# Kernel tuning notes

Measured on AMD Instinct MI355X. Metric: run time of the kernel, lower is better.

## Reference

```python
import jax, jax.numpy as jnp
import numpy as np

B, N, H = 8, 128, 512   # batch, num_sent (n == m required by the 'all' branch), hidden_size
D = 2 * H               # bi-LSTM output dim
SCALE = 0.05


def setup_inputs() -> dict:
    key = jax.random.key(0)
    ks = jax.random.split(key, 24)
    p = lambda k, shape: (jax.random.normal(k, shape, dtype=jnp.float32) * SCALE)
    return {
        "x0_enc": jax.random.normal(ks[0], (B, N, D), dtype=jnp.float32),
        "x1_enc": jax.random.normal(ks[1], (B, N, D), dtype=jnp.float32),
        # concat_attention
        "Wc1": p(ks[2], (D, H)), "Wc2": p(ks[3], (D, H)), "vc": p(ks[4], (H,)),
        # bilinear_attention
        "Wb": p(ks[5], (D, D)),
        # dot_attention x2 (separate params)
        "Wd1": p(ks[6], (D, H)), "vd1": p(ks[7], (H,)),
        "Wd2": p(ks[8], (D, H)), "vd2": p(ks[9], (H,)),
        # minus_attention (Ws/vs are unused in forward)
        "Wm": p(ks[10], (D, H)), "vm": p(ks[11], (H,)),
        # aggregation_layer
        "Wq": p(ks[12], (D, H)), "vq": p(ks[13], (H,)),
        "Wp1": p(ks[14], (2 * D, H)), "Wp2": p(ks[15], (D, H)), "vp": p(ks[16], (H,)),
        "Wpred": p(ks[17], (2 * D, 2)), "bpred": jnp.zeros((2,), dtype=jnp.float32),
    }


def _dot_att(x, y, Wd, vd):
    # sjt[b,m,n] = vd . tanh(Wd(x[b,n] * y[b,m]))  -- pairwise elementwise product + MLP
    z = jnp.tanh(jnp.einsum("bnd,bmd,dh->bmnh", x, y, Wd))  # [B,m,n,H]
    s = jnp.einsum("bmnh,h->bmn", z, vd)
    a = jax.nn.softmax(s, axis=2)
    return jnp.einsum("bmn,bnd->bmd", a, x)


def _minus_att(x, y, Wm, vm):
    # Wm is linear, so Wm(x_n - y_m) = (x@Wm)_n - (y@Wm)_m
    a, b = x @ Wm, y @ Wm                                    # [B,n,H], [B,m,H]
    z = jnp.tanh(a[:, None, :, :] - b[:, :, None, :])        # [B,m,n,H]
    s = jnp.einsum("bmnh,h->bmn", z, vm)
    att = jax.nn.softmax(s, axis=2)
    return jnp.einsum("bmn,bnd->bmd", att, x)


def _concat_att(x, y, Wc1, Wc2, vc):
    a, b = x @ Wc1, y @ Wc2                                  # [B,n,H], [B,m,H]
    z = jnp.tanh(a[:, None, :, :] + b[:, :, None, :])        # [B,m,n,H]
    s = jnp.einsum("bmnh,h->bmn", z, vc)
    att = jax.nn.softmax(s, axis=2)
    return jnp.einsum("bmn,bnd->bmd", att, x)


def _bilinear_att(x, y, Wb):
    s = jnp.einsum("bmd,bnd->bmn", y, x @ Wb)
    att = jax.nn.softmax(s, axis=2)
    return jnp.einsum("bmn,bnd->bmd", att, x)


def reference(x0_enc, x1_enc, Wc1, Wc2, vc, Wb, Wd1, vd1, Wd2, vd2, Wm, vm,
              Wq, vq, Wp1, Wp2, vp, Wpred, bpred):
    x0, x1 = x0_enc, x1_enc
    # attention_fx('all')
    qtc = _concat_att(x0, x1, Wc1, Wc2, vc)
    qtb = _bilinear_att(x0, x1, Wb)
    qts = _dot_att(x0, x1, Wd1, vd1)
    qtd = _dot_att(x1, x0, Wd2, vd2)
    qtm = _minus_att(x0, x1, Wm, vm)
    agg_res = jnp.max(jnp.stack([x1, qts, qtc, qtd, qtb, qtm], axis=0), axis=0)  # [B,m,2H]
    # MultiAtt: dropout is identity in eval
    agg_rep = jnp.concatenate([x1, agg_res], axis=2)                             # [B,m,4H]
    # aggregation_layer
    sj = jnp.einsum("bnh,h->bn", jnp.tanh(x0 @ Wq), vq)
    rq = jnp.einsum("bn,bnd->bd", jax.nn.softmax(sj, axis=1), x0)                # [B,2H]
    t = agg_rep @ Wp1 + (rq @ Wp2)[:, None, :]                                   # [B,m,H]
    sp = jax.nn.softmax(jnp.einsum("bmh,h->bm", t, vp), axis=1)
    rp = jnp.einsum("bm,bmd->bd", sp, agg_rep)                                   # [B,4H]
    out = jax.nn.relu(rp @ Wpred + bpred)                                        # [B,2]
    return out
```

## Files before the change

kernel.cpp:

```cpp
#include <hip/hip_runtime.h>
#include <hip/hip_bf16.h>

static constexpr int Bc = 8, Nc = 128, Dc = 1024, Hc = 512;
static constexpr int BM = Bc * Nc;

typedef short short8 __attribute__((ext_vector_type(8)));
typedef float floatx4 __attribute__((ext_vector_type(4)));

__device__ __forceinline__ float fast_tanh(float x) {
  x = fminf(fmaxf(x, -15.f), 15.f);
  float e = __expf(2.f * x);
  return (e - 1.f) / (e + 1.f);
}

__device__ __forceinline__ ushort f2bf(float f) {
  unsigned u = __float_as_uint(f);
  u += 0x7FFFu + ((u >> 16) & 1u);
  return (ushort)(u >> 16);
}

__device__ __forceinline__ unsigned pk2(float a, float b) {
  return (unsigned)f2bf(a) | ((unsigned)f2bf(b) << 16);
}

__device__ __forceinline__ float block_sum256(float v, float* buf4) {
  #pragma unroll
  for (int o = 32; o; o >>= 1) v += __shfl_down(v, o, 64);
  const int w = threadIdx.x >> 6, lane = threadIdx.x & 63;
  if (lane == 0) buf4[w] = v;
  __syncthreads();
  return buf4[0] + buf4[1] + buf4[2] + buf4[3];
}

__global__ __launch_bounds__(256) void cvt_both(const float* __restrict__ x0,
                                                const float* __restrict__ x1,
                                                ushort* __restrict__ o0,
                                                ushort* __restrict__ o1) {
  int bi = blockIdx.x;
  const float* src = (bi < 512) ? x0 : x1;
  ushort* dst = (bi < 512) ? o0 : o1;
  int off = (bi & 511);
  int i = (off * 256 + threadIdx.x) * 8;
  float4 a = *reinterpret_cast<const float4*>(&src[i]);
  float4 b = *reinterpret_cast<const float4*>(&src[i + 4]);
  uint4 o;
  o.x = pk2(a.x, a.y); o.y = pk2(a.z, a.w);
  o.z = pk2(b.x, b.y); o.w = pk2(b.z, b.w);
  *reinterpret_cast<uint4*>(&dst[i]) = o;
}

struct TJobs {
  const float* src[7];
  ushort* dst[7];
  int J[7];
};
__global__ __launch_bounds__(256) void conv_transpose_multi(TJobs jobs) {
  const int job = blockIdx.z;
  const int J = jobs.J[job];
  const int h0 = blockIdx.y * 64;
  if (h0 >= J) return;
  const float* W = jobs.src[job];
  ushort* WT = jobs.dst[job];
  __shared__ float tile[64][65];
  const int d0 = blockIdx.x * 64;
  const int tid = threadIdx.x;
  #pragma unroll
  for (int i = 0; i < 16; i++) {
    int idx = tid + i * 256;
    int dd = idx >> 6, hh = idx & 63;
    tile[dd][hh] = W[(size_t)(d0 + dd) * J + h0 + hh];
  }
  __syncthreads();
  #pragma unroll
  for (int i = 0; i < 16; i++) {
    int idx = tid + i * 256;
    int hh = idx >> 6, dd = idx & 63;
    WT[(size_t)(h0 + hh) * Dc + d0 + dd] = f2bf(tile[dd][hh]);
  }
}

__global__ __launch_bounds__(256) void gemm_bt(const ushort* __restrict__ A,
                                               const ushort* __restrict__ BT,
                                               float* __restrict__ Cf,
                                               ushort* __restrict__ Cbf,
                                               int K, int ldc,
                                               size_t sA, size_t sB, size_t sC) {
  const int bz = blockIdx.z;
  A  += (size_t)bz * sA;
  BT += (size_t)bz * sB;
  const int m0 = blockIdx.y * 64, n0 = blockIdx.x * 64;
  __shared__ __align__(16) ushort Asl[64][40];
  __shared__ __align__(16) ushort Bsl[64][40];
  const int tid = threadIdx.x, wave = tid >> 6, lane = tid & 63;
  const int quad = lane >> 4, l15 = lane & 15;
  const int wr = (wave & 1) * 32, wc = (wave >> 1) * 32;
  const int rSt = tid >> 2, kSt8 = (tid & 3) * 8;
  floatx4 acc[2][2];
  #pragma unroll
  for (int i = 0; i < 2; i++)
    #pragma unroll
    for (int j = 0; j < 2; j++) acc[i][j] = (floatx4){0.f, 0.f, 0.f, 0.f};
  uint4 pa = *reinterpret_cast<const uint4*>(&A[(size_t)(m0 + rSt) * K + kSt8]);
  uint4 pb = *reinterpret_cast<const uint4*>(&BT[(size_t)(n0 + rSt) * K + kSt8]);
  for (int k0 = 0; k0 < K; k0 += 32) {
    *reinterpret_cast<uint4*>(&Asl[rSt][kSt8]) = pa;
    *reinterpret_cast<uint4*>(&Bsl[rSt][kSt8]) = pb;
    __syncthreads();
    if (k0 + 32 < K) {
      pa = *reinterpret_cast<const uint4*>(&A[(size_t)(m0 + rSt) * K + k0 + 32 + kSt8]);
      pb = *reinterpret_cast<const uint4*>(&BT[(size_t)(n0 + rSt) * K + k0 + 32 + kSt8]);
    }
    short8 af[2], bb[2];
    #pragma unroll
    for (int i = 0; i < 2; i++)
      af[i] = *reinterpret_cast<const short8*>(&Asl[wr + i * 16 + l15][quad * 8]);
    #pragma unroll
    for (int j = 0; j < 2; j++)
      bb[j] = *reinterpret_cast<const short8*>(&Bsl[wc + j * 16 + l15][quad * 8]);
    #pragma unroll
    for (int i = 0; i < 2; i++)
      #pragma unroll
      for (int j = 0; j < 2; j++)
        acc[i][j] = __builtin_amdgcn_mfma_f32_16x16x32_bf16(af[i], bb[j], acc[i][j], 0, 0, 0);
    __syncthreads();
  }
  if (Cbf) {
    #pragma unroll
    for (int i = 0; i < 2; i++)
      #pragma unroll
      for (int j = 0; j < 2; j++)
        #pragma unroll
        for (int r = 0; r < 4; r++) {
          int row = m0 + wr + i * 16 + quad * 4 + r;
          int col = n0 + wc + j * 16 + l15;
          Cbf[(size_t)bz * sC + (size_t)row * ldc + col] = f2bf(acc[i][j][r]);
        }
  } else {
    #pragma unroll
    for (int i = 0; i < 2; i++)
      #pragma unroll
      for (int j = 0; j < 2; j++)
        #pragma unroll
        for (int r = 0; r < 4; r++) {
          int row = m0 + wr + i * 16 + quad * 4 + r;
          int col = n0 + wc + j * 16 + l15;
          Cf[(size_t)bz * sC + (size_t)row * ldc + col] = acc[i][j][r];
        }
  }
}

__global__ __launch_bounds__(256, 2) void dot_scores_mfma3(const float* __restrict__ X0,
                                                           const float* __restrict__ X1,
                                                           const ushort* __restrict__ WdT1,
                                                           const ushort* __restrict__ WdT2,
                                                           const float* __restrict__ vd1,
                                                           const float* __restrict__ vd2,
                                                           float* __restrict__ Sd) {
  const int which = blockIdx.z;
  const float* X = which ? X1 : X0;
  const float* Y = which ? X0 : X1;
  const ushort* WdT = which ? WdT2 : WdT1;
  const float* v = which ? vd2 : vd1;
  float* S = Sd + (size_t)which * (BM * Nc);

  const int bm = blockIdx.y;
  const int b = bm >> 7;
  const int hBase = blockIdx.x * 256;
  const int tid = threadIdx.x;
  const int wave = tid >> 6, lane = tid & 63;
  const int quad = lane >> 4, l15 = lane & 15;
  const int wn = wave & 1, wh = wave >> 1;

  __shared__ __align__(16) char smraw[65536];
  ushort (*As0)[40] = (ushort(*)[40])(smraw);
  ushort (*As1)[40] = (ushort(*)[40])(smraw + 10240);
  ushort (*Bs0)[40] = (ushort(*)[40])(smraw + 20480);
  ushort (*Bs1)[40] = (ushort(*)[40])(smraw + 40960);
  float* yl = (float*)(smraw + 61440);
  float (*red)[33] = (float(*)[33])(smraw);

  for (int i = tid; i < Dc; i += 256) yl[i] = Y[(size_t)bm * Dc + i];

  floatx4 acc[4][8];
  #pragma unroll
  for (int i = 0; i < 4; i++)
    #pragma unroll
    for (int j = 0; j < 8; j++) acc[i][j] = (floatx4){0.f, 0.f, 0.f, 0.f};

  const float* Xb = X + (size_t)b * Nc * Dc;
  const int nSt = tid >> 2;
  const int kSt4 = (tid & 3) * 4;
  const int kSt8 = (tid & 3) * 8;

  auto stage = [&](int k0, ushort (*Asb)[40], ushort (*Bsb)[40]) {
    #pragma unroll
    for (int u2 = 0; u2 < 4; u2++) {
      const int n = (u2 >> 1) * 64 + nSt;
      const int kc = (u2 & 1) * 16 + kSt4;
      float4 xv = *reinterpret_cast<const float4*>(&Xb[(size_t)n * Dc + k0 + kc]);
      float4 yv = *reinterpret_cast<const float4*>(&yl[k0 + kc]);
      uint2 o;
      o.x = pk2(xv.x * yv.x, xv.y * yv.y);
      o.y = pk2(xv.z * yv.z, xv.w * yv.w);
      *reinterpret_cast<uint2*>(&Asb[n][kc]) = o;
    }
    #pragma unroll
    for (int r = 0; r < 4; r++)
      *reinterpret_cast<uint4*>(&Bsb[r * 64 + nSt][kSt8]) =
          *reinterpret_cast<const uint4*>(&WdT[(size_t)(hBase + r * 64 + nSt) * Dc + k0 + kSt8]);
  };

  auto mfma_step = [&](ushort (*Asb)[40], ushort (*Bsb)[40]) {
    short8 af[4], bfr[8];
    #pragma unroll
    for (int i = 0; i < 4; i++)
      af[i] = *reinterpret_cast<const short8*>(&Asb[wn * 64 + i * 16 + l15][quad * 8]);
    #pragma unroll
    for (int j = 0; j < 8; j++)
      bfr[j] = *reinterpret_cast<const short8*>(&Bsb[wh * 128 + j * 16 + l15][quad * 8]);
    #pragma unroll
    for (int i = 0; i < 4; i++)
      #pragma unroll
      for (int j = 0; j < 8; j++)
        acc[i][j] = __builtin_amdgcn_mfma_f32_16x16x32_bf16(af[i], bfr[j], acc[i][j], 0, 0, 0);
  };

  __syncthreads();
  stage(0, As0, Bs0);
  __syncthreads();
  #pragma unroll 1
  for (int s = 0; s < 32; s += 2) {
    if (s + 1 < 32) stage((s + 1) * 32, As1, Bs1);
    mfma_step(As0, Bs0);
    __syncthreads();
    if (s + 2 < 32) stage((s + 2) * 32, As0, Bs0);
    mfma_step(As1, Bs1);
    __syncthreads();
  }

  float vv[8];
  #pragma unroll
  for (int j = 0; j < 8; j++) vv[j] = v[hBase + wh * 128 + j * 16 + l15];
  #pragma unroll
  for (int i = 0; i < 4; i++)
    #pragma unroll
    for (int r = 0; r < 4; r++) {
      float p = 0.f;
      #pragma unroll
      for (int j = 0; j < 8; j++) p = fmaf(vv[j], fast_tanh(acc[i][j][r]), p);
      red[wn * 64 + i * 16 + quad * 4 + r][wh * 16 + l15] = p;
    }
  __syncthreads();
  if (tid < 128) {
    float s = 0.f;
    #pragma unroll
    for (int c = 0; c < 32; c++) s += red[tid][c];
    atomicAdd(&S[(size_t)bm * Nc + tid], s);
  }
}

__global__ __launch_bounds__(256) void addtanh_tiled(const float* __restrict__ Arow,
                                                     const float* __restrict__ Brow,
                                                     const float* __restrict__ v,
                                                     float sign, float* __restrict__ S,
                                                     int rs) {
  const int nt = blockIdx.x, mt = blockIdx.y, b = blockIdx.z;
  __shared__ __align__(16) float at[16][516];
  __shared__ __align__(16) float bt2[16][516];
  __shared__ __align__(16) float vl[512];
  const int tid = threadIdx.x;
  #pragma unroll
  for (int p = 0; p < 8; p++) {
    int idx = p * 256 + tid;
    int r = idx >> 7, c4 = (idx & 127) * 4;
    *reinterpret_cast<float4*>(&at[r][c4]) =
        *reinterpret_cast<const float4*>(&Arow[(size_t)(b * Nc + nt * 16 + r) * rs + c4]);
    *reinterpret_cast<float4*>(&bt2[r][c4]) =
        *reinterpret_cast<const float4*>(&Brow[(size_t)(b * Nc + mt * 16 + r) * rs + c4]);
  }
  if (tid < 128)
    *reinterpret_cast<float4*>(&vl[tid * 4]) = *reinterpret_cast<const float4*>(&v[tid * 4]);
  __syncthreads();
  const int m = tid >> 4, n = tid & 15;
  float acc = 0.f;
  #pragma unroll 4
  for (int c = 0; c < 512; c += 4) {
    float4 av = *reinterpret_cast<const float4*>(&at[n][c]);
    float4 bv = *reinterpret_cast<const float4*>(&bt2[m][c]);
    float4 vv = *reinterpret_cast<const float4*>(&vl[c]);
    acc = fmaf(vv.x, fast_tanh(fmaf(sign, bv.x, av.x)), acc);
    acc = fmaf(vv.y, fast_tanh(fmaf(sign, bv.y, av.y)), acc);
    acc = fmaf(vv.z, fast_tanh(fmaf(sign, bv.z, av.z)), acc);
    acc = fmaf(vv.w, fast_tanh(fmaf(sign, bv.w, av.w)), acc);
  }
  S[(size_t)(b * Nc + mt * 16 + m) * Nc + nt * 16 + n] = acc;
}

__global__ __launch_bounds__(128) void softmax128(float* __restrict__ S) {
  const int row = blockIdx.x;
  const int tid = threadIdx.x;
  float x = S[(size_t)row * 128 + tid];
  __shared__ float mbuf[2], sbuf[2];
  float mx = x;
  #pragma unroll
  for (int o = 32; o; o >>= 1) mx = fmaxf(mx, __shfl_down(mx, o, 64));
  if ((tid & 63) == 0) mbuf[tid >> 6] = mx;
  __syncthreads();
  mx = fmaxf(mbuf[0], mbuf[1]);
  float e = __expf(x - mx);
  float sm = e;
  #pragma unroll
  for (int o = 32; o; o >>= 1) sm += __shfl_down(sm, o, 64);
  if ((tid & 63) == 0) sbuf[tid >> 6] = sm;
  __syncthreads();
  sm = sbuf[0] + sbuf[1];
  S[(size_t)row * 128 + tid] = e / sm;
}

#define FMA4(acc, s, v)                  \
  acc.x = fmaf(s, v.x, acc.x);           \
  acc.y = fmaf(s, v.y, acc.y);           \
  acc.z = fmaf(s, v.z, acc.z);           \
  acc.w = fmaf(s, v.w, acc.w)

__global__ __launch_bounds__(256) void agg_max(const float* __restrict__ x0,
                                               const float* __restrict__ x1,
                                               const float* __restrict__ Sc,
                                               const float* __restrict__ Sb,
                                               const float* __restrict__ Sd1,
                                               const float* __restrict__ Sd2,
                                               const float* __restrict__ Sm,
                                               float* __restrict__ agg) {
  const int bm = blockIdx.x;
  const int b = bm >> 7;
  const int tid = threadIdx.x;
  __shared__ float w[5][128];
  if (tid < 128) {
    w[0][tid] = Sc[(size_t)bm * Nc + tid];
    w[1][tid] = Sb[(size_t)bm * Nc + tid];
    w[2][tid] = Sd1[(size_t)bm * Nc + tid];
    w[3][tid] = Sd2[(size_t)bm * Nc + tid];
    w[4][tid] = Sm[(size_t)bm * Nc + tid];
  }
  __syncthreads();
  const int d0 = tid * 4;
  float4 qc = {0, 0, 0, 0}, qb = {0, 0, 0, 0}, qs = {0, 0, 0, 0};
  float4 qd = {0, 0, 0, 0}, qm = {0, 0, 0, 0};
  const float* X0b = x0 + (size_t)b * Nc * Dc;
  const float* X1b = x1 + (size_t)b * Nc * Dc;
  for (int n = 0; n < Nc; n++) {
    float4 xv = *reinterpret_cast<const float4*>(&X0b[(size_t)n * Dc + d0]);
    float4 yv = *reinterpret_cast<const float4*>(&X1b[(size_t)n * Dc + d0]);
    float wc = w[0][n], wb = w[1][n], ws = w[2][n], wd = w[3][n], wm = w[4][n];
    FMA4(qc, wc, xv);
    FMA4(qb, wb, xv);
    FMA4(qs, ws, xv);
    FMA4(qd, wd, yv);
    FMA4(qm, wm, xv);
  }
  float4 x1v = *reinterpret_cast<const float4*>(&x1[(size_t)bm * Dc + d0]);
  float4 r;
  r.x = fmaxf(x1v.x, fmaxf(fmaxf(qs.x, qc.x), fmaxf(fmaxf(qd.x, qb.x), qm.x)));
  r.y = fmaxf(x1v.y, fmaxf(fmaxf(qs.y, qc.y), fmaxf(fmaxf(qd.y, qb.y), qm.y)));
  r.z = fmaxf(x1v.z, fmaxf(fmaxf(qs.z, qc.z), fmaxf(fmaxf(qd.z, qb.z), qm.z)));
  r.w = fmaxf(x1v.w, fmaxf(fmaxf(qs.w, qc.w), fmaxf(fmaxf(qd.w, qb.w), qm.w)));
  *reinterpret_cast<float4*>(&agg[(size_t)bm * Dc + d0]) = r;
}

__global__ __launch_bounds__(64) void compute_u(const float* __restrict__ Wp1,
                                                const float* __restrict__ vp,
                                                float* __restrict__ u) {
  const int d2 = blockIdx.x;
  const int tid = threadIdx.x;
  float p = 0.f;
  #pragma unroll
  for (int h = tid; h < Hc; h += 64) p = fmaf(Wp1[(size_t)d2 * Hc + h], vp[h], p);
  #pragma unroll
  for (int o = 32; o; o >>= 1) p += __shfl_down(p, o, 64);
  if (tid == 0) u[d2] = p;
}

__global__ __launch_bounds__(256) void final_scores(const float* __restrict__ x1,
                                                    const float* __restrict__ agg,
                                                    const float* __restrict__ u,
                                                    float* __restrict__ score) {
  const int bm = blockIdx.x;
  const int tid = threadIdx.x;
  float p = 0.f;
  #pragma unroll
  for (int d = tid; d < Dc; d += 256)
    p = fmaf(x1[(size_t)bm * Dc + d], u[d], fmaf(agg[(size_t)bm * Dc + d], u[Dc + d], p));
  __shared__ float buf4[4];
  p = block_sum256(p, buf4);
  if (tid == 0) score[bm] = p;
}

__global__ __launch_bounds__(256) void final_out(const float* __restrict__ x1,
                                                 const float* __restrict__ agg,
                                                 const float* __restrict__ score,
                                                 const float* __restrict__ Wpred,
                                                 const float* __restrict__ bpred,
                                                 float* __restrict__ out) {
  const int b = blockIdx.x;
  const int tid = threadIdx.x;
  __shared__ float spL[128];
  __shared__ float mbuf[2], sbuf[2];
  if (tid < 128) {
    float x = score[b * Nc + tid];
    float mx = x;
    #pragma unroll
    for (int o = 32; o; o >>= 1) mx = fmaxf(mx, __shfl_down(mx, o, 64));
    if ((tid & 63) == 0) mbuf[tid >> 6] = mx;
  }
  __syncthreads();
  if (tid < 128) {
    float x = score[b * Nc + tid];
    float mx = fmaxf(mbuf[0], mbuf[1]);
    float e = __expf(x - mx);
    float sm = e;
    #pragma unroll
    for (int o = 32; o; o >>= 1) sm += __shfl_down(sm, o, 64);
    if ((tid & 63) == 0) sbuf[tid >> 6] = sm;
    spL[tid] = e;
  }
  __syncthreads();
  const float inv = 1.f / (sbuf[0] + sbuf[1]);
  const int d2 = tid * 8;
  float w0[8], w1[8];
  #pragma unroll
  for (int i = 0; i < 8; i++) {
    w0[i] = Wpred[(size_t)(d2 + i) * 2 + 0];
    w1[i] = Wpred[(size_t)(d2 + i) * 2 + 1];
  }
  const float* src = (d2 < Dc) ? (x1 + (size_t)b * Nc * Dc + d2)
                               : (agg + (size_t)b * Nc * Dc + (d2 - Dc));
  float p0 = 0.f, p1 = 0.f;
  for (int m = 0; m < Nc; m++) {
    float s = spL[m] * inv;
    const float* r = src + (size_t)m * Dc;
    #pragma unroll
    for (int i = 0; i < 8; i++) {
      float sc = s * r[i];
      p0 = fmaf(sc, w0[i], p0);
      p1 = fmaf(sc, w1[i], p1);
    }
  }
  #pragma unroll
  for (int o = 32; o; o >>= 1) {
    p0 += __shfl_down(p0, o, 64);
    p1 += __shfl_down(p1, o, 64);
  }
  __shared__ float r0[4], r1[4];
  const int w = tid >> 6, lane = tid & 63;
  if (lane == 0) { r0[w] = p0; r1[w] = p1; }
  __syncthreads();
  if (tid == 0) {
    float q0 = r0[0] + r0[1] + r0[2] + r0[3] + bpred[0];
    float q1 = r1[0] + r1[1] + r1[2] + r1[3] + bpred[1];
    out[b * 2 + 0] = fmaxf(q0, 0.f);
    out[b * 2 + 1] = fmaxf(q1, 0.f);
  }
}

extern "C" void kernel_launch(void* const* d_in, const int* in_sizes, int n_in,
                              void* d_out, int out_size, void* d_ws, size_t ws_size,
                              hipStream_t stream) {
  const float* x0    = (const float*)d_in[0];
  const float* x1    = (const float*)d_in[1];
  const float* Wc1   = (const float*)d_in[2];
  const float* Wc2   = (const float*)d_in[3];
  const float* vc    = (const float*)d_in[4];
  const float* Wb    = (const float*)d_in[5];
  const float* Wd1   = (const float*)d_in[6];
  const float* vd1   = (const float*)d_in[7];
  const float* Wd2   = (const float*)d_in[8];
  const float* vd2   = (const float*)d_in[9];
  const float* Wm    = (const float*)d_in[10];
  const float* vm    = (const float*)d_in[11];
  const float* Wp1   = (const float*)d_in[14];
  const float* vp    = (const float*)d_in[16];
  const float* Wpred = (const float*)d_in[17];
  const float* bpred = (const float*)d_in[18];
  float* out = (float*)d_out;

  float* ws = (float*)d_ws;
  float* C1     = ws;
  float* C2     = C1 + 1048576;
  float* sc     = C2 + 1048576;
  float* sb     = sc + 131072;
  float* sd1    = sb + 131072;
  float* sd2    = sd1 + 131072;
  float* smv    = sd2 + 131072;
  float* u      = smv + 131072;
  float* score2 = u + 2048;
  ushort* x0bf  = (ushort*)(score2 + 1024);
  ushort* x1bf  = x0bf + 1048576;
  ushort* W1T   = x1bf + 1048576;
  ushort* W2T   = W1T + 1048576;
  ushort* WbT   = W2T + 1048576;
  ushort* xWbbf = WbT + 1048576;
  ushort* wdT1  = xWbbf + 1048576;
  ushort* wdT2  = wdT1 + 524288;
  float* agg    = C1;

  cvt_both<<<1024, 256, 0, stream>>>(x0, x1, x0bf, x1bf);
  TJobs tj;
  tj.src[0] = Wd1; tj.dst[0] = wdT1;            tj.J[0] = Hc;
  tj.src[1] = Wd2; tj.dst[1] = wdT2;            tj.J[1] = Hc;
  tj.src[2] = Wc1; tj.dst[2] = W1T;             tj.J[2] = Hc;
  tj.src[3] = Wm;  tj.dst[3] = W1T + 512 * Dc;  tj.J[3] = Hc;
  tj.src[4] = Wc2; tj.dst[4] = W2T;             tj.J[4] = Hc;
  tj.src[5] = Wm;  tj.dst[5] = W2T + 512 * Dc;  tj.J[5] = Hc;
  tj.src[6] = Wb;  tj.dst[6] = WbT;             tj.J[6] = Dc;
  conv_transpose_multi<<<dim3(16, 16, 7), 256, 0, stream>>>(tj);

  gemm_bt<<<dim3(16, 16, 1), 256, 0, stream>>>(x0bf, W1T, C1, nullptr, Dc, 1024, 0, 0, 0);
  gemm_bt<<<dim3(16, 16, 1), 256, 0, stream>>>(x1bf, W2T, C2, nullptr, Dc, 1024, 0, 0, 0);
  gemm_bt<<<dim3(16, 16, 1), 256, 0, stream>>>(x0bf, WbT, nullptr, xWbbf, Dc, 1024, 0, 0, 0);
  gemm_bt<<<dim3(2, 2, 8), 256, 0, stream>>>(x1bf, xWbbf, sb, nullptr, Dc, 128,
                                             131072, 131072, 16384);

  addtanh_tiled<<<dim3(8, 8, 8), 256, 0, stream>>>(C1, C2, vc, 1.f, sc, 1024);
  addtanh_tiled<<<dim3(8, 8, 8), 256, 0, stream>>>(C1 + 512, C2 + 512, vm, -1.f, smv, 1024);

  (void)hipMemsetAsync(sd1, 0, 2 * 131072 * sizeof(float), stream);
  dot_scores_mfma3<<<dim3(2, BM, 2), 256, 0, stream>>>(x0, x1, wdT1, wdT2, vd1, vd2, sd1);

  softmax128<<<5 * BM, 128, 0, stream>>>(sc);

  agg_max<<<BM, 256, 0, stream>>>(x0, x1, sc, sb, sd1, sd2, smv, agg);

  compute_u<<<2 * Dc, 64, 0, stream>>>(Wp1, vp, u);
  final_scores<<<BM, 256, 0, stream>>>(x1, agg, u, score2);
  final_out<<<Bc, 256, 0, stream>>>(x1, agg, score2, Wpred, bpred, out);
}
```

Measured before the change: 701.1 us.

## Switch MFMA pipeline from bf16 to fp16 and stage dot-attention inputs in half

All bf16 conversions and MFMA calls become fp16 (cvt_pkrtz packing, f16 MFMA). The dot-attention score kernel now reads the pre-converted half-precision x0/x1 and forms the pairwise product with packed half8 multiplies, replacing fp32 loads and per-element conversion during staging. This halves its global read traffic and cuts conversion ALU work. The two addtanh launches are also merged into one grid. Risks: fp16 range and overflow in products and the xWb intermediate, and a different rounding error profile than bf16.

Measured after the change: 651.0 us. 7.1% less time.

```diff
diff --git a/kernel.cpp b/kernel.cpp
--- a/kernel.cpp
+++ b/kernel.cpp
@@ -4,7 +4,8 @@
 static constexpr int Bc = 8, Nc = 128, Dc = 1024, Hc = 512;
 static constexpr int BM = Bc * Nc;
 
-typedef short short8 __attribute__((ext_vector_type(8)));
+typedef _Float16 half8 __attribute__((ext_vector_type(8)));
+typedef __fp16 fp16x2 __attribute__((ext_vector_type(2)));
 typedef float floatx4 __attribute__((ext_vector_type(4)));
 
 __device__ __forceinline__ float fast_tanh(float x) {
@@ -13,14 +14,14 @@
   return (e - 1.f) / (e + 1.f);
 }
 
-__device__ __forceinline__ ushort f2bf(float f) {
-  unsigned u = __float_as_uint(f);
-  u += 0x7FFFu + ((u >> 16) & 1u);
-  return (ushort)(u >> 16);
-}
-
-__device__ __forceinline__ unsigned pk2(float a, float b) {
-  return (unsigned)f2bf(a) | ((unsigned)f2bf(b) << 16);
+__device__ __forceinline__ unsigned pkh2(float a, float b) {
+  fp16x2 h = __builtin_amdgcn_cvt_pkrtz(a, b);
+  return __builtin_bit_cast(unsigned, h);
+}
+
+__device__ __forceinline__ ushort f2h(float f) {
+  _Float16 h = (_Float16)f;
+  return __builtin_bit_cast(ushort, h);
 }
 
 __device__ __forceinline__ float block_sum256(float v, float* buf4) {
@@ -44,8 +45,8 @@
   float4 a = *reinterpret_cast<const float4*>(&src[i]);
   float4 b = *reinterpret_cast<const float4*>(&src[i + 4]);
   uint4 o;
-  o.x = pk2(a.x, a.y); o.y = pk2(a.z, a.w);
-  o.z = pk2(b.x, b.y); o.w = pk2(b.z, b.w);
+  o.x = pkh2(a.x, a.y); o.y = pkh2(a.z, a.w);
+  o.z = pkh2(b.x, b.y); o.w = pkh2(b.z, b.w);
   *reinterpret_cast<uint4*>(&dst[i]) = o;
 }
 
@@ -75,14 +76,14 @@
   for (int i = 0; i < 16; i++) {
     int idx = tid + i * 256;
     int hh = idx >> 6, dd = idx & 63;
-    WT[(size_t)(h0 + hh) * Dc + d0 + dd] = f2bf(tile[dd][hh]);
+    WT[(size_t)(h0 + hh) * Dc + d0 + dd] = f2h(tile[dd][hh]);
   }
 }
 
 __global__ __launch_bounds__(256) void gemm_bt(const ushort* __restrict__ A,
                                                const ushort* __restrict__ BT,
                                                float* __restrict__ Cf,
-                                               ushort* __restrict__ Cbf,
+                                               ushort* __restrict__ Ch,
                                                int K, int ldc,
                                                size_t sA, size_t sB, size_t sC) {
   const int bz = blockIdx.z;
@@ -110,21 +111,21 @@
       pa = *reinterpret_cast<const uint4*>(&A[(size_t)(m0 + rSt) * K + k0 + 32 + kSt8]);
       pb = *reinterpret_cast<const uint4*>(&BT[(size_t)(n0 + rSt) * K + k0 + 32 + kSt8]);
     }
-    short8 af[2], bb[2];
+    half8 af[2], bb[2];
     #pragma unroll
     for (int i = 0; i < 2; i++)
-      af[i] = *reinterpret_cast<const short8*>(&Asl[wr + i * 16 + l15][quad * 8]);
+      af[i] = *reinterpret_cast<const half8*>(&Asl[wr + i * 16 + l15][quad * 8]);
     #pragma unroll
     for (int j = 0; j < 2; j++)
-      bb[j] = *reinterpret_cast<const short8*>(&Bsl[wc + j * 16 + l15][quad * 8]);
+      bb[j] = *reinterpret_cast<const half8*>(&Bsl[wc + j * 16 + l15][quad * 8]);
     #pragma unroll
     for (int i = 0; i < 2; i++)
       #pragma unroll
       for (int j = 0; j < 2; j++)
-        acc[i][j] = __builtin_amdgcn_mfma_f32_16x16x32_bf16(af[i], bb[j], acc[i][j], 0, 0, 0);
+        acc[i][j] = __builtin_amdgcn_mfma_f32_16x16x32_f16(af[i], bb[j], acc[i][j], 0, 0, 0);
     __syncthreads();
   }
-  if (Cbf) {
+  if (Ch) {
     #pragma unroll
     for (int i = 0; i < 2; i++)
       #pragma unroll
@@ -133,7 +134,7 @@
         for (int r = 0; r < 4; r++) {
           int row = m0 + wr + i * 16 + quad * 4 + r;
           int col = n0 + wc + j * 16 + l15;
-          Cbf[(size_t)bz * sC + (size_t)row * ldc + col] = f2bf(acc[i][j][r]);
+          Ch[(size_t)bz * sC + (size_t)row * ldc + col] = f2h(acc[i][j][r]);
         }
   } else {
     #pragma unroll
@@ -149,16 +150,16 @@
   }
 }
 
-__global__ __launch_bounds__(256, 2) void dot_scores_mfma3(const float* __restrict__ X0,
-                                                           const float* __restrict__ X1,
+__global__ __launch_bounds__(256, 2) void dot_scores_mfma4(const ushort* __restrict__ X0h,
+                                                           const ushort* __restrict__ X1h,
                                                            const ushort* __restrict__ WdT1,
                                                            const ushort* __restrict__ WdT2,
                                                            const float* __restrict__ vd1,
                                                            const float* __restrict__ vd2,
                                                            float* __restrict__ Sd) {
   const int which = blockIdx.z;
-  const float* X = which ? X1 : X0;
-  const float* Y = which ? X0 : X1;
+  const ushort* Xh = which ? X1h : X0h;
+  const ushort* Yh = which ? X0h : X1h;
   const ushort* WdT = which ? WdT2 : WdT1;
   const float* v = which ? vd2 : vd1;
   float* S = Sd + (size_t)which * (BM * Nc);
@@ -176,10 +177,14 @@
   ushort (*As1)[40] = (ushort(*)[40])(smraw + 10240);
   ushort (*Bs0)[40] = (ushort(*)[40])(smraw + 20480);
   ushort (*Bs1)[40] = (ushort(*)[40])(smraw + 40960);
-  float* yl = (float*)(smraw + 61440);
+  ushort* ylh = (ushort*)(smraw + 61440);
   float (*red)[33] = (float(*)[33])(smraw);
 
-  for (int i = tid; i < Dc; i += 256) yl[i] = Y[(size_t)bm * Dc + i];
+  {
+    const uint* Yrow = (const uint*)(Yh + (size_t)bm * Dc);
+    uint* dst = (uint*)ylh;
+    for (int i = tid; i < Dc / 2; i += 256) dst[i] = Yrow[i];
+  }
 
   floatx4 acc[4][8];
   #pragma unroll
@@ -187,22 +192,18 @@
     #pragma unroll
     for (int j = 0; j < 8; j++) acc[i][j] = (floatx4){0.f, 0.f, 0.f, 0.f};
 
-  const float* Xb = X + (size_t)b * Nc * Dc;
+  const ushort* Xb = Xh + (size_t)b * Nc * Dc;
   const int nSt = tid >> 2;
-  const int kSt4 = (tid & 3) * 4;
   const int kSt8 = (tid & 3) * 8;
 
   auto stage = [&](int k0, ushort (*Asb)[40], ushort (*Bsb)[40]) {
-    #pragma unroll
-    for (int u2 = 0; u2 < 4; u2++) {
-      const int n = (u2 >> 1) * 64 + nSt;
-      const int kc = (u2 & 1) * 16 + kSt4;
-      float4 xv = *reinterpret_cast<const float4*>(&Xb[(size_t)n * Dc + k0 + kc]);
-      float4 yv = *reinterpret_cast<const float4*>(&yl[k0 + kc]);
-      uint2 o;
-      o.x = pk2(xv.x * yv.x, xv.y * yv.y);
-      o.y = pk2(xv.z * yv.z, xv.w * yv.w);
-      *reinterpret_cast<uint2*>(&Asb[n][kc]) = o;
+    half8 yv = *reinterpret_cast<const half8*>(&ylh[k0 + kSt8]);
+    #pragma unroll
+    for (int p = 0; p < 2; p++) {
+      const int n = p * 64 + nSt;
+      half8 xv = *reinterpret_cast<const half8*>(&Xb[(size_t)n * Dc + k0 + kSt8]);
+      half8 prod = xv * yv;
+      *reinterpret_cast<half8*>(&Asb[n][kSt8]) = prod;
     }
     #pragma unroll
     for (int r = 0; r < 4; r++)
@@ -211,18 +212,18 @@
   };
 
   auto mfma_step = [&](ushort (*Asb)[40], ushort (*Bsb)[40]) {
-    short8 af[4], bfr[8];
+    half8 af[4], bfr[8];
     #pragma unroll
     for (int i = 0; i < 4; i++)
-      af[i] = *reinterpret_cast<const short8*>(&Asb[wn * 64 + i * 16 + l15][quad * 8]);
+      af[i] = *reinterpret_cast<const half8*>(&Asb[wn * 64 + i * 16 + l15][quad * 8]);
     #pragma unroll
     for (int j = 0; j < 8; j++)
-      bfr[j] = *reinterpret_cast<const short8*>(&Bsb[wh * 128 + j * 16 + l15][quad * 8]);
+      bfr[j] = *reinterpret_cast<const half8*>(&Bsb[wh * 128 + j * 16 + l15][quad * 8]);
     #pragma unroll
     for (int i = 0; i < 4; i++)
       #pragma unroll
       for (int j = 0; j < 8; j++)
-        acc[i][j] = __builtin_amdgcn_mfma_f32_16x16x32_bf16(af[i], bfr[j], acc[i][j], 0, 0, 0);
+        acc[i][j] = __builtin_amdgcn_mfma_f32_16x16x32_f16(af[i], bfr[j], acc[i][j], 0, 0, 0);
   };
 
   __syncthreads();
@@ -259,12 +260,19 @@
   }
 }
 
-__global__ __launch_bounds__(256) void addtanh_tiled(const float* __restrict__ Arow,
-                                                     const float* __restrict__ Brow,
-                                                     const float* __restrict__ v,
-                                                     float sign, float* __restrict__ S,
-                                                     int rs) {
-  const int nt = blockIdx.x, mt = blockIdx.y, b = blockIdx.z;
+__global__ __launch_bounds__(256) void addtanh_tiled2(const float* __restrict__ C1,
+                                                      const float* __restrict__ C2,
+                                                      const float* __restrict__ vc,
+                                                      const float* __restrict__ vm,
+                                                      float* __restrict__ Sc,
+                                                      float* __restrict__ Sm) {
+  const int nt = blockIdx.x, mt = blockIdx.y;
+  const int which = blockIdx.z >> 3, b = blockIdx.z & 7;
+  const float* Arow = C1 + which * 512;
+  const float* Brow = C2 + which * 512;
+  const float* v = which ? vm : vc;
+  const float sign = which ? -1.f : 1.f;
+  float* S = which ? Sm : Sc;
   __shared__ __align__(16) float at[16][516];
   __shared__ __align__(16) float bt2[16][516];
   __shared__ __align__(16) float vl[512];
@@ -274,9 +282,9 @@
     int idx = p * 256 + tid;
     int r = idx >> 7, c4 = (idx & 127) * 4;
     *reinterpret_cast<float4*>(&at[r][c4]) =
-        *reinterpret_cast<const float4*>(&Arow[(size_t)(b * Nc + nt * 16 + r) * rs + c4]);
+        *reinterpret_cast<const float4*>(&Arow[(size_t)(b * Nc + nt * 16 + r) * 1024 + c4]);
     *reinterpret_cast<float4*>(&bt2[r][c4]) =
-        *reinterpret_cast<const float4*>(&Brow[(size_t)(b * Nc + mt * 16 + r) * rs + c4]);
+        *reinterpret_cast<const float4*>(&Brow[(size_t)(b * Nc + mt * 16 + r) * 1024 + c4]);
   }
   if (tid < 128)
     *reinterpret_cast<float4*>(&vl[tid * 4]) = *reinterpret_cast<const float4*>(&v[tid * 4]);
@@ -493,17 +501,17 @@
   float* smv    = sd2 + 131072;
   float* u      = smv + 131072;
   float* score2 = u + 2048;
-  ushort* x0bf  = (ushort*)(score2 + 1024);
-  ushort* x1bf  = x0bf + 1048576;
-  ushort* W1T   = x1bf + 1048576;
+  ushort* x0h   = (ushort*)(score2 + 1024);
+  ushort* x1h   = x0h + 1048576;
+  ushort* W1T   = x1h + 1048576;
   ushort* W2T   = W1T + 1048576;
   ushort* WbT   = W2T + 1048576;
-  ushort* xWbbf = WbT + 1048576;
-  ushort* wdT1  = xWbbf + 1048576;
+  ushort* xWbh  = WbT + 1048576;
+  ushort* wdT1  = xWbh + 1048576;
   ushort* wdT2  = wdT1 + 524288;
   float* agg    = C1;
 
-  cvt_both<<<1024, 256, 0, stream>>>(x0, x1, x0bf, x1bf);
+  cvt_both<<<1024, 256, 0, stream>>>(x0, x1, x0h, x1h);
   TJobs tj;
   tj.src[0] = Wd1; tj.dst[0] = wdT1;            tj.J[0] = Hc;
   tj.src[1] = Wd2; tj.dst[1] = wdT2;            tj.J[1] = Hc;
@@ -514,17 +522,16 @@
   tj.src[6] = Wb;  tj.dst[6] = WbT;             tj.J[6] = Dc;
   conv_transpose_multi<<<dim3(16, 16, 7), 256, 0, stream>>>(tj);
 
-  gemm_bt<<<dim3(16, 16, 1), 256, 0, stream>>>(x0bf, W1T, C1, nullptr, Dc, 1024, 0, 0, 0);
-  gemm_bt<<<dim3(16, 16, 1), 256, 0, stream>>>(x1bf, W2T, C2, nullptr, Dc, 1024, 0, 0, 0);
-  gemm_bt<<<dim3(16, 16, 1), 256, 0, stream>>>(x0bf, WbT, nullptr, xWbbf, Dc, 1024, 0, 0, 0);
-  gemm_bt<<<dim3(2, 2, 8), 256, 0, stream>>>(x1bf, xWbbf, sb, nullptr, Dc, 128,
+  gemm_bt<<<dim3(16, 16, 1), 256, 0, stream>>>(x0h, W1T, C1, nullptr, Dc, 1024, 0, 0, 0);
+  gemm_bt<<<dim3(16, 16, 1), 256, 0, stream>>>(x1h, W2T, C2, nullptr, Dc, 1024, 0, 0, 0);
+  gemm_bt<<<dim3(16, 16, 1), 256, 0, stream>>>(x0h, WbT, nullptr, xWbh, Dc, 1024, 0, 0, 0);
+  gemm_bt<<<dim3(2, 2, 8), 256, 0, stream>>>(x1h, xWbh, sb, nullptr, Dc, 128,
                                              131072, 131072, 16384);
 
-  addtanh_tiled<<<dim3(8, 8, 8), 256, 0, stream>>>(C1, C2, vc, 1.f, sc, 1024);
-  addtanh_tiled<<<dim3(8, 8, 8), 256, 0, stream>>>(C1 + 512, C2 + 512, vm, -1.f, smv, 1024);
+  addtanh_tiled2<<<dim3(8, 8, 16), 256, 0, stream>>>(C1, C2, vc, vm, sc, smv);
 
   (void)hipMemsetAsync(sd1, 0, 2 * 131072 * sizeof(float), stream);
-  dot_scores_mfma3<<<dim3(2, BM, 2), 256, 0, stream>>>(x0, x1, wdT1, wdT2, vd1, vd2, sd1);
+  dot_scores_mfma4<<<dim3(2, BM, 2), 256, 0, stream>>>(x0h, x1h, wdT1, wdT2, vd1, vd2, sd1);
 
   softmax128<<<5 * BM, 128, 0, stream>>>(sc);
 
```
